# Kernel optimization log

Measured on AMD Instinct MI355X. Metric: run time of the kernel, lower is better.

Reference implementation:

```python
import jax, jax.numpy as jnp
import numpy as np

B, S, K, N = 4, 2048, 4096, 16384

def setup_inputs() -> dict:
    key = jax.random.key(0)
    k1, k2, k3, k4 = jax.random.split(key, 4)
    x = jax.random.normal(k1, (B, S, K), dtype=jnp.float32)
    weight_data = jax.random.randint(k2, (N, K), -127, 128, dtype=jnp.int32)  # holds int8-range values
    scale = jax.random.uniform(k3, (N, 1), dtype=jnp.float32, minval=0.001, maxval=0.02)
    bias = jax.random.normal(k4, (N,), dtype=jnp.float32)
    return {"x": x, "weight_data": weight_data, "scale": scale, "bias": bias}

def reference(x, weight_data, scale, bias):
    x_shape = x.shape
    x_flat = x.reshape(-1, K)                      # [M, K]
    max_val = jnp.max(jnp.abs(x_flat), axis=1, keepdims=True)  # [M, 1]
    scale_x = max_val / 127.0
    scale_x = jnp.where(scale_x == 0, jnp.float32(1.0), scale_x)
    x_int8 = jnp.clip(jnp.round(x_flat / scale_x), -127, 127).astype(jnp.int8)
    w_int8 = weight_data.astype(jnp.int8)          # [N, K]
    # int8 GEMM with int32 accumulation (torch._int_mm equivalent)
    y_int32 = jax.lax.dot_general(
        x_int8, w_int8.T,
        dimension_numbers=(((1,), (0,)), ((), ())),
        preferred_element_type=jnp.int32)           # [M, N]
    y = y_int32.astype(jnp.float32) * scale_x * scale.reshape(1, -1)
    y = y.reshape(x_shape[0], x_shape[1], N)
    y = y + bias
    return y
```

## Files before the change

### kernel.cpp

```cpp
#include <hip/hip_runtime.h>
#include <cstdint>

#define MDIM 8192
#define KDIM 4096
#define NDIM 16384

#define BM 256
#define BN 256
#define BKB 64
#define NT (KDIM / BKB)
#define NBUF 4

typedef int v4i __attribute__((ext_vector_type(4)));

__device__ __forceinline__ void gload_lds16(const void* g, void* l) {
    __builtin_amdgcn_global_load_lds(
        (const __attribute__((address_space(1))) int*)g,
        (__attribute__((address_space(3))) int*)l, 16, 0, 0);
}

__global__ __launch_bounds__(256) void conv_w(const int4* __restrict__ w,
                                              int* __restrict__ wq) {
    int g = blockIdx.x * 256 + threadIdx.x;
    int4 v = w[g];
    unsigned p = (unsigned)(v.x & 255) | ((unsigned)(v.y & 255) << 8) |
                 ((unsigned)(v.z & 255) << 16) | ((unsigned)(v.w & 255) << 24);
    wq[g] = (int)p;
}

__global__ __launch_bounds__(256) void quant_rows(const float* __restrict__ x,
                                                  int* __restrict__ xq32,
                                                  float* __restrict__ sx) {
    const int row = blockIdx.x;
    const int t = threadIdx.x;
    const float4* xr = (const float4*)(x + (size_t)row * KDIM);

    float4 v[4];
    float amax = 0.f;
#pragma unroll
    for (int p = 0; p < 4; ++p) {
        v[p] = xr[p * 256 + t];
        amax = fmaxf(amax, fmaxf(fmaxf(fabsf(v[p].x), fabsf(v[p].y)),
                                 fmaxf(fabsf(v[p].z), fabsf(v[p].w))));
    }
#pragma unroll
    for (int off = 32; off > 0; off >>= 1)
        amax = fmaxf(amax, __shfl_down(amax, off));
    __shared__ float wmax[4];
    int wave = t >> 6, lane = t & 63;
    if (lane == 0) wmax[wave] = amax;
    __syncthreads();
    float m = fmaxf(fmaxf(wmax[0], wmax[1]), fmaxf(wmax[2], wmax[3]));

    float inv = (m > 0.f) ? 127.f / m : 0.f;
    if (t == 0) {
        float s = m / 127.f;
        sx[row] = (s == 0.f) ? 1.f : s;
    }

    int* out = xq32 + (size_t)row * (KDIM / 4);
#pragma unroll
    for (int p = 0; p < 4; ++p) {
        int q0 = (int)rintf(v[p].x * inv); q0 = max(-127, min(127, q0));
        int q1 = (int)rintf(v[p].y * inv); q1 = max(-127, min(127, q1));
        int q2 = (int)rintf(v[p].z * inv); q2 = max(-127, min(127, q2));
        int q3 = (int)rintf(v[p].w * inv); q3 = max(-127, min(127, q3));
        unsigned pk = (unsigned)(q0 & 255) | ((unsigned)(q1 & 255) << 8) |
                      ((unsigned)(q2 & 255) << 16) | ((unsigned)(q3 & 255) << 24);
        out[p * 256 + t] = (int)pk;
    }
}

__global__ __launch_bounds__(512, 2) void gemm_i8(const signed char* __restrict__ xq,
                                                  const signed char* __restrict__ wq,
                                                  const float* __restrict__ sx,
                                                  const float* __restrict__ scale,
                                                  const float* __restrict__ bias,
                                                  float* __restrict__ y) {
    __shared__ __align__(16) signed char lds_a[NBUF][BM * BKB];
    __shared__ __align__(16) signed char lds_b[NBUF][BN * BKB];

    const int tid  = threadIdx.x;
    const int lane = tid & 63;
    const int wave = tid >> 6;
    const int l16  = lane & 15;
    const int quad = lane >> 4;
    const int wm   = wave >> 2;
    const int wn   = wave & 3;

    int lin = blockIdx.y * gridDim.x + blockIdx.x;
    lin = (lin & 7) * ((MDIM / BM) * (NDIM / BN) / 8) + (lin >> 3);
    const int tileN = (lin & (NDIM / BN - 1)) * BN;
    const int tileM = (lin >> 6) * BM;

    const int srow = tid >> 2;
    const int scol = ((tid & 3) << 4) ^ (((srow >> 1) & 3) << 4);
    const signed char* gA0 = xq + (size_t)(tileM + srow) * KDIM + scol;
    const signed char* gA1 = gA0 + (size_t)128 * KDIM;
    const signed char* gB0 = wq + (size_t)(tileN + srow) * KDIM + scol;
    const signed char* gB1 = gB0 + (size_t)128 * KDIM;
    const int lo = tid << 4;

    const int rcol = (quad << 4) ^ (((l16 >> 1) & 3) << 4);
    const int aoff = (wm * 128 + l16) * BKB + rcol;
    const int boff = (wn * 64 + l16) * BKB + rcol;

    v4i acc[8][4] = {};

#define STAGE_A(GOFF, BUF) do {                                               \
        gload_lds16(gA0 + (GOFF), &lds_a[BUF][lo]);                           \
        gload_lds16(gA1 + (GOFF), &lds_a[BUF][lo + 8192]); } while (0)
#define STAGE_B(GOFF, BUF) do {                                               \
        gload_lds16(gB0 + (GOFF), &lds_b[BUF][lo]);                           \
        gload_lds16(gB1 + (GOFF), &lds_b[BUF][lo + 8192]); } while (0)

#define KTILE(BC_, DO_PF_, PFOFF_) do {                                       \
    v4i af_[4], bf_[4], ag_[4];                                               \
    _Pragma("unroll")                                                         \
    for (int i_ = 0; i_ < 4; ++i_)                                            \
        af_[i_] = *(const v4i*)(&lds_a[BC_][0] + aoff + i_ * 1024);           \
    _Pragma("unroll")                                                         \
    for (int j_ = 0; j_ < 4; ++j_)                                            \
        bf_[j_] = *(const v4i*)(&lds_b[BC_][0] + boff + j_ * 1024);           \
    if (DO_PF_) STAGE_A(PFOFF_, ((BC_) + 3) & 3);                             \
    __builtin_amdgcn_s_barrier();                                             \
    asm volatile("s_waitcnt lgkmcnt(0)" ::: "memory");                        \
    __builtin_amdgcn_sched_barrier(0);                                        \
    __builtin_amdgcn_s_setprio(1);                                            \
    _Pragma("unroll")                                                         \
    for (int i_ = 0; i_ < 4; ++i_)                                            \
        _Pragma("unroll")                                                     \
        for (int j_ = 0; j_ < 4; ++j_)                                        \
            acc[i_][j_] = __builtin_amdgcn_mfma_i32_16x16x64_i8(              \
                af_[i_], bf_[j_], acc[i_][j_], 0, 0, 0);                      \
    __builtin_amdgcn_s_setprio(0);                                            \
    __builtin_amdgcn_s_barrier();                                             \
    _Pragma("unroll")                                                         \
    for (int i_ = 0; i_ < 4; ++i_)                                            \
        ag_[i_] = *(const v4i*)(&lds_a[BC_][0] + aoff + (4 + i_) * 1024);     \
    if (DO_PF_) STAGE_B(PFOFF_, ((BC_) + 3) & 3);                             \
    __builtin_amdgcn_s_barrier();                                             \
    asm volatile("s_waitcnt lgkmcnt(0)" ::: "memory");                        \
    __builtin_amdgcn_sched_barrier(0);                                        \
    __builtin_amdgcn_s_setprio(1);                                            \
    _Pragma("unroll")                                                         \
    for (int i_ = 0; i_ < 4; ++i_)                                            \
        _Pragma("unroll")                                                     \
        for (int j_ = 0; j_ < 4; ++j_)                                        \
            acc[4 + i_][j_] = __builtin_amdgcn_mfma_i32_16x16x64_i8(          \
                ag_[i_], bf_[j_], acc[4 + i_][j_], 0, 0, 0);                  \
    __builtin_amdgcn_s_setprio(0);                                            \
} while (0)

#define VMW(N) asm volatile("s_waitcnt vmcnt(" #N ")" ::: "memory")

    STAGE_A((size_t)0 * BKB, 0); STAGE_B((size_t)0 * BKB, 0);
    STAGE_A((size_t)1 * BKB, 1); STAGE_B((size_t)1 * BKB, 1);
    STAGE_A((size_t)2 * BKB, 2); STAGE_B((size_t)2 * BKB, 2);
    VMW(8);
    __builtin_amdgcn_s_barrier();

    for (int g = 0; g < 15; ++g) {
        const size_t kb = (size_t)g * 4 * BKB;
#pragma unroll
        for (int i = 0; i < 4; ++i) {
            KTILE(i, true, kb + (size_t)(i + 3) * BKB);
            VMW(8);
            __builtin_amdgcn_s_barrier();
        }
    }

    KTILE(0, true, (size_t)63 * BKB);
    VMW(8);
    __builtin_amdgcn_s_barrier();
    KTILE(1, false, 0);
    VMW(4);
    __builtin_amdgcn_s_barrier();
    KTILE(2, false, 0);
    VMW(0);
    __builtin_amdgcn_s_barrier();
    KTILE(3, false, 0);

    float sxv[8][4];
#pragma unroll
    for (int i = 0; i < 8; ++i)
#pragma unroll
        for (int r = 0; r < 4; ++r)
            sxv[i][r] = sx[tileM + wm * 128 + i * 16 + quad * 4 + r];

#pragma unroll
    for (int j = 0; j < 4; ++j) {
        const int n = tileN + wn * 64 + j * 16 + l16;
        const float scn = scale[n];
        const float bsn = bias[n];
#pragma unroll
        for (int i = 0; i < 8; ++i) {
            const size_t mrow = (size_t)(tileM + wm * 128 + i * 16 + quad * 4);
#pragma unroll
            for (int r = 0; r < 4; ++r)
                y[(mrow + r) * NDIM + n] = (float)acc[i][j][r] * sxv[i][r] * scn + bsn;
        }
    }
#undef STAGE_A
#undef STAGE_B
#undef KTILE
#undef VMW
}

extern "C" void kernel_launch(void* const* d_in, const int* in_sizes, int n_in,
                              void* d_out, int out_size, void* d_ws, size_t ws_size,
                              hipStream_t stream) {
    const float* x      = (const float*)d_in[0];
    const int*   wdat   = (const int*)d_in[1];
    const float* scale  = (const float*)d_in[2];
    const float* bias   = (const float*)d_in[3];
    float* y = (float*)d_out;

    signed char* wq = (signed char*)d_ws;
    signed char* xq = wq + (size_t)NDIM * KDIM;
    float*       sx = (float*)(xq + (size_t)MDIM * KDIM);

    conv_w<<<(NDIM * (size_t)KDIM) / 4 / 256, 256, 0, stream>>>((const int4*)wdat,
                                                                (int*)wq);
    quant_rows<<<MDIM, 256, 0, stream>>>(x, (int*)xq, sx);

    dim3 grid(NDIM / BN, MDIM / BM);
    gemm_i8<<<grid, 512, 0, stream>>>(xq, wq, sx, scale, bias, y);
}
```

Baseline: 1.342 ms.

## Double-buffer MFMA fragments in registers and halve barriers per K-tile

```diff
diff --git a/kernel.cpp b/kernel.cpp
--- a/kernel.cpp
+++ b/kernel.cpp
@@ -9,7 +9,6 @@
 #define BN 256
 #define BKB 64
 #define NT (KDIM / BKB)
-#define NBUF 4
 
 typedef int v4i __attribute__((ext_vector_type(4)));
 
@@ -77,8 +76,8 @@
                                                   const float* __restrict__ scale,
                                                   const float* __restrict__ bias,
                                                   float* __restrict__ y) {
-    __shared__ __align__(16) signed char lds_a[NBUF][BM * BKB];
-    __shared__ __align__(16) signed char lds_b[NBUF][BN * BKB];
+    __shared__ __align__(16) signed char lds_a[4][BM * BKB];
+    __shared__ __align__(16) signed char lds_b[4][BN * BKB];
 
     const int tid  = threadIdx.x;
     const int lane = tid & 63;
@@ -106,6 +105,7 @@
     const int boff = (wn * 64 + l16) * BKB + rcol;
 
     v4i acc[8][4] = {};
+    v4i A0[4], B0[4], A1[4], B1[4];
 
 #define STAGE_A(GOFF, BUF) do {                                               \
         gload_lds16(gA0 + (GOFF), &lds_a[BUF][lo]);                           \
@@ -114,72 +114,68 @@
         gload_lds16(gB0 + (GOFF), &lds_b[BUF][lo]);                           \
         gload_lds16(gB1 + (GOFF), &lds_b[BUF][lo + 8192]); } while (0)
 
-#define KTILE(BC_, DO_PF_, PFOFF_) do {                                       \
-    v4i af_[4], bf_[4], ag_[4];                                               \
+#define VMW(N) asm volatile("s_waitcnt vmcnt(" #N ")" ::: "memory")
+
+#define TILE(BC_, CA_, CB_, NA_, NB_, DO_PF_, PFOFF_, DO_NEXT_, DO_SYNC_, VMN_) do { \
+    v4i vg_[4];                                                               \
+            \
     _Pragma("unroll")                                                         \
     for (int i_ = 0; i_ < 4; ++i_)                                            \
-        af_[i_] = *(const v4i*)(&lds_a[BC_][0] + aoff + i_ * 1024);           \
-    _Pragma("unroll")                                                         \
-    for (int j_ = 0; j_ < 4; ++j_)                                            \
-        bf_[j_] = *(const v4i*)(&lds_b[BC_][0] + boff + j_ * 1024);           \
+        vg_[i_] = *(const v4i*)(&lds_a[BC_][0] + aoff + (4 + i_) * 1024);     \
     if (DO_PF_) STAGE_A(PFOFF_, ((BC_) + 3) & 3);                             \
-    __builtin_amdgcn_s_barrier();                                             \
-    asm volatile("s_waitcnt lgkmcnt(0)" ::: "memory");                        \
-    __builtin_amdgcn_sched_barrier(0);                                        \
     __builtin_amdgcn_s_setprio(1);                                            \
     _Pragma("unroll")                                                         \
     for (int i_ = 0; i_ < 4; ++i_)                                            \
         _Pragma("unroll")                                                     \
         for (int j_ = 0; j_ < 4; ++j_)                                        \
             acc[i_][j_] = __builtin_amdgcn_mfma_i32_16x16x64_i8(              \
-                af_[i_], bf_[j_], acc[i_][j_], 0, 0, 0);                      \
+                CA_[i_], CB_[j_], acc[i_][j_], 0, 0, 0);                      \
     __builtin_amdgcn_s_setprio(0);                                            \
-    __builtin_amdgcn_s_barrier();                                             \
-    _Pragma("unroll")                                                         \
-    for (int i_ = 0; i_ < 4; ++i_)                                            \
-        ag_[i_] = *(const v4i*)(&lds_a[BC_][0] + aoff + (4 + i_) * 1024);     \
+       \
+    if (DO_SYNC_) { VMW(VMN_); __builtin_amdgcn_s_barrier(); }                \
+    if (DO_NEXT_) {                                                           \
+        _Pragma("unroll")                                                     \
+        for (int i_ = 0; i_ < 4; ++i_)                                        \
+            NA_[i_] = *(const v4i*)(&lds_a[((BC_) + 1) & 3][0] + aoff + i_ * 1024); \
+        _Pragma("unroll")                                                     \
+        for (int j_ = 0; j_ < 4; ++j_)                                        \
+            NB_[j_] = *(const v4i*)(&lds_b[((BC_) + 1) & 3][0] + boff + j_ * 1024); \
+    }                                                                         \
     if (DO_PF_) STAGE_B(PFOFF_, ((BC_) + 3) & 3);                             \
-    __builtin_amdgcn_s_barrier();                                             \
-    asm volatile("s_waitcnt lgkmcnt(0)" ::: "memory");                        \
-    __builtin_amdgcn_sched_barrier(0);                                        \
     __builtin_amdgcn_s_setprio(1);                                            \
     _Pragma("unroll")                                                         \
     for (int i_ = 0; i_ < 4; ++i_)                                            \
         _Pragma("unroll")                                                     \
         for (int j_ = 0; j_ < 4; ++j_)                                        \
             acc[4 + i_][j_] = __builtin_amdgcn_mfma_i32_16x16x64_i8(          \
-                ag_[i_], bf_[j_], acc[4 + i_][j_], 0, 0, 0);                  \
+                vg_[i_], CB_[j_], acc[4 + i_][j_], 0, 0, 0);                  \
     __builtin_amdgcn_s_setprio(0);                                            \
+    if (DO_SYNC_) __builtin_amdgcn_s_barrier();                               \
 } while (0)
-
-#define VMW(N) asm volatile("s_waitcnt vmcnt(" #N ")" ::: "memory")
 
     STAGE_A((size_t)0 * BKB, 0); STAGE_B((size_t)0 * BKB, 0);
     STAGE_A((size_t)1 * BKB, 1); STAGE_B((size_t)1 * BKB, 1);
     STAGE_A((size_t)2 * BKB, 2); STAGE_B((size_t)2 * BKB, 2);
     VMW(8);
     __builtin_amdgcn_s_barrier();
+#pragma unroll
+    for (int i = 0; i < 4; ++i) {
+        A0[i] = *(const v4i*)(&lds_a[0][0] + aoff + i * 1024);
+        B0[i] = *(const v4i*)(&lds_b[0][0] + boff + i * 1024);
+    }
 
     for (int g = 0; g < 15; ++g) {
         const size_t kb = (size_t)g * 4 * BKB;
-#pragma unroll
-        for (int i = 0; i < 4; ++i) {
-            KTILE(i, true, kb + (size_t)(i + 3) * BKB);
-            VMW(8);
-            __builtin_amdgcn_s_barrier();
-        }
-    }
-
-    KTILE(0, true, (size_t)63 * BKB);
-    VMW(8);
-    __builtin_amdgcn_s_barrier();
-    KTILE(1, false, 0);
-    VMW(4);
-    __builtin_amdgcn_s_barrier();
-    KTILE(2, false, 0);
-    VMW(0);
-    __builtin_amdgcn_s_barrier();
-    KTILE(3, false, 0);
+        TILE(0, A0, B0, A1, B1, true, kb + (size_t)3 * BKB, true, true, 6);
+        TILE(1, A1, B1, A0, B0, true, kb + (size_t)4 * BKB, true, true, 6);
+        TILE(2, A0, B0, A1, B1, true, kb + (size_t)5 * BKB, true, true, 6);
+        TILE(3, A1, B1, A0, B0, true, kb + (size_t)6 * BKB, true, true, 6);
+    }
+
+    TILE(0, A0, B0, A1, B1, true, (size_t)63 * BKB, true, true, 6);
+    TILE(1, A1, B1, A0, B0, false, 0, true, true, 4);
+    TILE(2, A0, B0, A1, B1, false, 0, true, true, 0);
+    TILE(3, A1, B1, A0, B0, false, 0, false, false, 0);
 
     float sxv[8][4];
 #pragma unroll
@@ -203,7 +199,7 @@
     }
 #undef STAGE_A
 #undef STAGE_B
-#undef KTILE
+#undef TILE
 #undef VMW
 }
 
```

Measured after the change: 1.379 ms. 1.03x slower.
